# Optimization experiments

Hardware: AMD Instinct MI355X
Metric: run time of the kernel (lower is better)

Reference implementation:

```python
import jax, jax.numpy as jnp
import numpy as np

TOTAL_WORDS = 10000
EMB = 100
SEQ = 80
UNITS = 64


def setup_inputs() -> dict:
    key = jax.random.key(0)
    ks = jax.random.split(key, 10)
    B = 16384
    tokens = jax.random.randint(ks[0], (B, SEQ), 0, TOTAL_WORDS, dtype=jnp.int32)
    s = 0.05
    emb = jax.random.normal(ks[1], (TOTAL_WORDS, EMB), jnp.float32) * s
    Wx0 = jax.random.normal(ks[2], (EMB, UNITS), jnp.float32) * s
    Wh0 = jax.random.normal(ks[3], (UNITS, UNITS), jnp.float32) * s
    b0 = jnp.zeros((UNITS,), jnp.float32)
    Wx1 = jax.random.normal(ks[4], (UNITS, UNITS), jnp.float32) * s
    Wh1 = jax.random.normal(ks[5], (UNITS, UNITS), jnp.float32) * s
    b1 = jnp.zeros((UNITS,), jnp.float32)
    Wout = jax.random.normal(ks[6], (UNITS, 1), jnp.float32) * s
    bout = jnp.zeros((1,), jnp.float32)
    return {"tokens": tokens, "emb": emb, "Wx0": Wx0, "Wh0": Wh0, "b0": b0,
            "Wx1": Wx1, "Wh1": Wh1, "b1": b1, "Wout": Wout, "bout": bout}


def reference(tokens, emb, Wx0, Wh0, b0, Wx1, Wh1, b1, Wout, bout):
    # Embedding lookup: [B, SEQ, EMB]
    x = emb[tokens]
    B = tokens.shape[0]
    # time-major for scan: [SEQ, B, EMB]
    xt = jnp.transpose(x, (1, 0, 2))
    h0 = jnp.zeros((B, UNITS), x.dtype)
    h1 = jnp.zeros((B, UNITS), x.dtype)

    def step(carry, x_t):
        h0, h1 = carry
        # SimpleRNNCell (inference, dropout inactive): h' = tanh(x Wx + h Wh + b)
        h0n = jnp.tanh(x_t @ Wx0 + h0 @ Wh0 + b0)
        h1n = jnp.tanh(h0n @ Wx1 + h1 @ Wh1 + b1)
        return (h0n, h1n), None

    (h0, h1), _ = jax.lax.scan(step, (h0, h1), xt)
    logits = h1 @ Wout + bout  # [B, 1]
    return jax.nn.sigmoid(logits)
```

## Files before the change

kernel.cpp:

```cpp
#include <hip/hip_runtime.h>

#define TOTAL_WORDS 10000
#define EMB 100
#define SEQ 80
#define UNITS 64
#define BATCH 16384


typedef _Float16 f16x8 __attribute__((ext_vector_type(8)));
typedef _Float16 h2    __attribute__((ext_vector_type(2)));
typedef __fp16   fp16x2r __attribute__((ext_vector_type(2)));
typedef float    f32x4 __attribute__((ext_vector_type(4)));
typedef unsigned int u32;
typedef u32      u32x4 __attribute__((ext_vector_type(4)));

#define PIN(x) asm volatile("" : "+v"(x))

__device__ __forceinline__ u32 tanh_pk(float x, float y) {
    h2 v = __builtin_bit_cast(h2, __builtin_amdgcn_cvt_pkrtz(x, y));
    const _Float16 c3 = (_Float16)(-0.33333333f);
    const _Float16 c5 = (_Float16)(0.13333333f);
    h2 x2 = v * v;
    h2 p  = x2 * c5 + c3;
    h2 x3 = x2 * v;
    h2 r  = x3 * p + v;
    return __builtin_bit_cast(u32, r);
}

__device__ __forceinline__ f16x8 tanh_frag(f32x4 a, f32x4 b) {
    u32x4 w;
    w.x = tanh_pk(a[0], a[1]);
    w.y = tanh_pk(a[2], a[3]);
    w.z = tanh_pk(b[0], b[1]);
    w.w = tanh_pk(b[2], b[3]);
    return __builtin_bit_cast(f16x8, w);
}

__global__ void prep_kernel(const float* __restrict__ emb,
                            const float* __restrict__ Wx0,
                            const float* __restrict__ b0,
                            const float* __restrict__ Wh0,
                            const float* __restrict__ Wx1,
                            const float* __restrict__ Wh1,
                            float* __restrict__ embW,
                            _Float16* __restrict__ wfrags) {
    int b = blockIdx.x;
    if (b < 250) {
        __shared__ float wx[EMB * UNITS];
        for (int i = threadIdx.x; i < EMB * UNITS; i += 256)
            wx[i] = Wx0[i];
        __syncthreads();
        const int u = threadIdx.x & 63;
        const int wvi = threadIdx.x >> 6;
        const int vbase = b * 40 + wvi * 10;
        const float bias = b0[u];
        float acc[10];
#pragma unroll
        for (int i = 0; i < 10; ++i) acc[i] = bias;
        const float* er = emb + vbase * EMB;
#pragma unroll 4
        for (int k = 0; k < EMB; ++k) {
            float wxv = wx[k * UNITS + u];
#pragma unroll
            for (int i = 0; i < 10; ++i)
                acc[i] = fmaf(er[i * EMB + k], wxv, acc[i]);
        }
#pragma unroll
        for (int i = 0; i < 10; ++i)
            embW[(vbase + i) * UNITS + u] = acc[i];
    } else {
        int e = (b - 250) * 256 + threadIdx.x;
        int mat = e >> 12;
        int ee = e & 4095;
        int f = ee >> 9;
        int mt = f >> 1, kf = f & 1;
        int rr = ee & 511;
        int l = rr >> 3, j = rr & 7;
        int k = kf * 32 + (l >> 4) * 8 + j;
        int mm = l & 15;
        int col = 32 * (mt >> 1) + 8 * (mm >> 2) + 4 * (mt & 1) + (mm & 3);
        const float* W = (mat == 0) ? Wh0 : (mat == 1) ? Wx1 : Wh1;
        wfrags[e] = (_Float16)W[k * UNITS + col];
    }
}

#define MF(A, B, C) __builtin_amdgcn_mfma_f32_16x16x32_f16(A, B, C, 0, 0, 0)

#define RNN_ITER(EJ, TOK3)                                                    \
    {                                                                         \
                       \
        f32x4 c0 = MF(wh[0][0], h1f0, b1v[0]);                                \
        f32x4 c1 = MF(wh[1][0], h1f0, b1v[1]);                                \
        f32x4 c2 = MF(wh[2][0], h1f0, b1v[2]);                                \
        f32x4 c3 = MF(wh[3][0], h1f0, b1v[3]);                                \
                              \
        f32x4 a0 = MF(w0[0][0], h0f0, EJ[0]);                                 \
        f32x4 a1 = MF(w0[1][0], h0f0, EJ[1]);                                 \
        f32x4 a2 = MF(w0[2][0], h0f0, EJ[2]);                                 \
        f32x4 a3 = MF(w0[3][0], h0f0, EJ[3]);                                 \
                                                        \
        c0 = MF(wh[0][1], h1f1, c0);                                          \
        c1 = MF(wh[1][1], h1f1, c1);                                          \
        c2 = MF(wh[2][1], h1f1, c2);                                          \
        c3 = MF(wh[3][1], h1f1, c3);                                          \
                       \
        {                                                                     \
            const f32x4* pe = embq + (size_t)(TOK3) * 16;                     \
            EJ[0] = pe[0]; EJ[1] = pe[1]; EJ[2] = pe[8]; EJ[3] = pe[9];       \
        }                                                                     \
                                                        \
        a0 = MF(w0[0][1], h0f1, a0);                                          \
        a1 = MF(w0[1][1], h0f1, a1);                                          \
        a2 = MF(w0[2][1], h0f1, a2);                                          \
        a3 = MF(w0[3][1], h0f1, a3);                                          \
                                       \
        c0 = MF(wx[0][0], h0f0, c0);                                          \
        c1 = MF(wx[1][0], h0f0, c1);                                          \
        c2 = MF(wx[2][0], h0f0, c2);                                          \
        c3 = MF(wx[3][0], h0f0, c3);                                          \
                                  \
        f16x8 nh0f0 = tanh_frag(a0, a1);                                      \
        f16x8 nh0f1 = tanh_frag(a2, a3);                                      \
                                       \
        c0 = MF(wx[0][1], h0f1, c0);                                          \
        c1 = MF(wx[1][1], h0f1, c1);                                          \
        c2 = MF(wx[2][1], h0f1, c2);                                          \
        c3 = MF(wx[3][1], h0f1, c3);                                          \
        h0f0 = nh0f0; h0f1 = nh0f1;                                           \
        h1f0 = tanh_frag(c0, c1);                                             \
        h1f1 = tanh_frag(c2, c3);                                             \
    }

__global__ __launch_bounds__(64, 1) void rnn_mfma_kernel(
    const int*      __restrict__ tokens,
    const float*    __restrict__ embW,
    const _Float16* __restrict__ wfrags,
    const float*    __restrict__ b1,
    const float*    __restrict__ Wout,
    const float*    __restrict__ bout,
    float*          __restrict__ out) {
    const int l = threadIdx.x;
    const int q = l >> 4;
    const int n = l & 15;
    const int row0 = blockIdx.x * 16;

    const f16x8* wf8 = (const f16x8*)wfrags;
    f16x8 w0[4][2], wx[4][2], wh[4][2];
#pragma unroll
    for (int t = 0; t < 4; ++t)
#pragma unroll
        for (int kf = 0; kf < 2; ++kf) {
            w0[t][kf] = wf8[(t * 2 + kf) * 64 + l];
            wx[t][kf] = wf8[(8 + t * 2 + kf) * 64 + l];
            wh[t][kf] = wf8[(16 + t * 2 + kf) * 64 + l];
        }

    const f32x4* b1v4 = (const f32x4*)b1;
    f32x4 b1v[4];
    b1v[0] = b1v4[0 + 2 * q];
    b1v[1] = b1v4[1 + 2 * q];
    b1v[2] = b1v4[8 + 2 * q];
    b1v[3] = b1v4[9 + 2 * q];

#pragma unroll
    for (int t = 0; t < 4; ++t) {
        PIN(w0[t][0]); PIN(w0[t][1]);
        PIN(wx[t][0]); PIN(wx[t][1]);
        PIN(wh[t][0]); PIN(wh[t][1]);
        PIN(b1v[t]);
    }

    const f32x4* embq = (const f32x4*)embW + 2 * q;
    const int tokbase = (row0 + n) * SEQ;

    int4 cur = *(const int4*)&tokens[tokbase];
    int4 nxt = *(const int4*)&tokens[tokbase + 4];

    f16x8 h0f0, h0f1, h1f0, h1f1;
    {
        const f32x4* pe = embq + (size_t)cur.x * 16;
        f32x4 p0 = pe[0], p1 = pe[1], p2 = pe[8], p3 = pe[9];
        h0f0 = tanh_frag(p0, p1);
        h0f1 = tanh_frag(p2, p3);
    }
#pragma unroll
    for (int j = 0; j < 8; ++j) { h1f0[j] = (_Float16)0.0f; h1f1[j] = (_Float16)0.0f; }

    f32x4 eA[4], eB[4];
    {
        const f32x4* pe;
        pe = embq + (size_t)cur.y * 16; eA[0]=pe[0]; eA[1]=pe[1]; eA[2]=pe[8]; eA[3]=pe[9];
        pe = embq + (size_t)cur.z * 16; eB[0]=pe[0]; eB[1]=pe[1]; eB[2]=pe[8]; eB[3]=pe[9];
    }

    for (int k = 0; k < SEQ / 4; ++k) {
        int off = (4 * k + 8 <= SEQ - 4) ? (4 * k + 8) : (SEQ - 4);
        int4 nn = *(const int4*)&tokens[tokbase + off];

        RNN_ITER(eA, cur.w)
        RNN_ITER(eB, nxt.x)
        RNN_ITER(eA, nxt.y)
        RNN_ITER(eB, nxt.z)

        cur = nxt;
        nxt = nn;
    }

    {
        f32x4 wo0 = ((const f32x4*)Wout)[2 * q];
        f32x4 wo1 = ((const f32x4*)Wout)[2 * q + 1];
        f32x4 wo2 = ((const f32x4*)Wout)[8 + 2 * q];
        f32x4 wo3 = ((const f32x4*)Wout)[8 + 2 * q + 1];
        float accv = 0.0f;
#pragma unroll
        for (int j = 0; j < 4; ++j) {
            accv = fmaf((float)h1f0[j],     wo0[j], accv);
            accv = fmaf((float)h1f0[4 + j], wo1[j], accv);
            accv = fmaf((float)h1f1[j],     wo2[j], accv);
            accv = fmaf((float)h1f1[4 + j], wo3[j], accv);
        }
        accv += __shfl_down(accv, 16);
        accv += __shfl_down(accv, 32);
        if (l < 16) {
            float z = accv + bout[0];
            out[row0 + n] = 1.0f / (1.0f + __expf(-z));
        }
    }
}

extern "C" void kernel_launch(void* const* d_in, const int* in_sizes, int n_in,
                              void* d_out, int out_size, void* d_ws, size_t ws_size,
                              hipStream_t stream) {
    const int*   tokens = (const int*)d_in[0];
    const float* emb    = (const float*)d_in[1];
    const float* Wx0    = (const float*)d_in[2];
    const float* Wh0    = (const float*)d_in[3];
    const float* b0     = (const float*)d_in[4];
    const float* Wx1    = (const float*)d_in[5];
    const float* Wh1    = (const float*)d_in[6];
    const float* b1     = (const float*)d_in[7];
    const float* Wout   = (const float*)d_in[8];
    const float* bout   = (const float*)d_in[9];
    float* out = (float*)d_out;

    float* embW = (float*)d_ws;
    _Float16* wfrags =
        (_Float16*)((char*)d_ws + (size_t)TOTAL_WORDS * UNITS * 4);

    prep_kernel<<<298, 256, 0, stream>>>(emb, Wx0, b0, Wh0, Wx1, Wh1,
                                         embW, wfrags);
    rnn_mfma_kernel<<<BATCH / 16, 64, 0, stream>>>(tokens, embW, wfrags,
                                                   b1, Wout, bout, out);
}
```

Before: 132.1 us.

## Split layer-1 accumulation into independent chains and deepen embedding prefetch

The layer-1 recurrence is split into two independent MFMA accumulation chains, one for h1·Wh1 with bias and one for h0·Wx1 from zero, which are summed before tanh. The three chains (layer 0, layer-1 recurrent, layer-1 input) are interleaved so consecutive MFMAs do not depend on each other, shortening the dependent chain per step. Embedding prefetch goes from two to four steps ahead using four register buffers, hiding more gather latency at the cost of extra VGPRs and one extra vector add per output.

New measurement: 140.7 us. +6.6%, slower.

```diff
diff --git a/kernel.cpp b/kernel.cpp
--- a/kernel.cpp
+++ b/kernel.cpp
@@ -86,49 +86,45 @@
 
 #define MF(A, B, C) __builtin_amdgcn_mfma_f32_16x16x32_f16(A, B, C, 0, 0, 0)
 
-#define RNN_ITER(EJ, TOK3)                                                    \
+#define RNN_ITER(EJ, TOK5)                                                    \
     {                                                                         \
-                       \
-        f32x4 c0 = MF(wh[0][0], h1f0, b1v[0]);                                \
-        f32x4 c1 = MF(wh[1][0], h1f0, b1v[1]);                                \
-        f32x4 c2 = MF(wh[2][0], h1f0, b1v[2]);                                \
-        f32x4 c3 = MF(wh[3][0], h1f0, b1v[3]);                                \
-                              \
-        f32x4 a0 = MF(w0[0][0], h0f0, EJ[0]);                                 \
-        f32x4 a1 = MF(w0[1][0], h0f0, EJ[1]);                                 \
-        f32x4 a2 = MF(w0[2][0], h0f0, EJ[2]);                                 \
-        f32x4 a3 = MF(w0[3][0], h0f0, EJ[3]);                                 \
-                                                        \
-        c0 = MF(wh[0][1], h1f1, c0);                                          \
-        c1 = MF(wh[1][1], h1f1, c1);                                          \
-        c2 = MF(wh[2][1], h1f1, c2);                                          \
-        c3 = MF(wh[3][1], h1f1, c3);                                          \
+               \
+        f32x4 ch0 = MF(wh[0][0], h1f0, b1v[0]);                               \
+        f32x4 a0  = MF(w0[0][0], h0f0, EJ[0]);                                \
+        f32x4 cx0 = MF(wx[0][0], h0f0, zv);                                   \
+        f32x4 ch1 = MF(wh[1][0], h1f0, b1v[1]);                               \
+        f32x4 a1  = MF(w0[1][0], h0f0, EJ[1]);                                \
+        f32x4 cx1 = MF(wx[1][0], h0f0, zv);                                   \
+        f32x4 ch2 = MF(wh[2][0], h1f0, b1v[2]);                               \
+        f32x4 a2  = MF(w0[2][0], h0f0, EJ[2]);                                \
+        f32x4 cx2 = MF(wx[2][0], h0f0, zv);                                   \
+        f32x4 ch3 = MF(wh[3][0], h1f0, b1v[3]);                               \
+        f32x4 a3  = MF(w0[3][0], h0f0, EJ[3]);                                \
+        f32x4 cx3 = MF(wx[3][0], h0f0, zv);                                   \
+                      \
+        ch0 = MF(wh[0][1], h1f1, ch0);                                        \
+        a0  = MF(w0[0][1], h0f1, a0);                                         \
+        cx0 = MF(wx[0][1], h0f1, cx0);                                        \
+        ch1 = MF(wh[1][1], h1f1, ch1);                                        \
+        a1  = MF(w0[1][1], h0f1, a1);                                         \
+        cx1 = MF(wx[1][1], h0f1, cx1);                                        \
+        ch2 = MF(wh[2][1], h1f1, ch2);                                        \
+        a2  = MF(w0[2][1], h0f1, a2);                                         \
+        cx2 = MF(wx[2][1], h0f1, cx2);                                        \
+        ch3 = MF(wh[3][1], h1f1, ch3);                                        \
+        a3  = MF(w0[3][1], h0f1, a3);                                         \
+        cx3 = MF(wx[3][1], h0f1, cx3);                                        \
                        \
         {                                                                     \
-            const f32x4* pe = embq + (size_t)(TOK3) * 16;                     \
+            const f32x4* pe = embq + (size_t)(TOK5) * 16;                     \
             EJ[0] = pe[0]; EJ[1] = pe[1]; EJ[2] = pe[8]; EJ[3] = pe[9];       \
         }                                                                     \
-                                                        \
-        a0 = MF(w0[0][1], h0f1, a0);                                          \
-        a1 = MF(w0[1][1], h0f1, a1);                                          \
-        a2 = MF(w0[2][1], h0f1, a2);                                          \
-        a3 = MF(w0[3][1], h0f1, a3);                                          \
-                                       \
-        c0 = MF(wx[0][0], h0f0, c0);                                          \
-        c1 = MF(wx[1][0], h0f0, c1);                                          \
-        c2 = MF(wx[2][0], h0f0, c2);                                          \
-        c3 = MF(wx[3][0], h0f0, c3);                                          \
-                                  \
+                 \
         f16x8 nh0f0 = tanh_frag(a0, a1);                                      \
         f16x8 nh0f1 = tanh_frag(a2, a3);                                      \
-                                       \
-        c0 = MF(wx[0][1], h0f1, c0);                                          \
-        c1 = MF(wx[1][1], h0f1, c1);                                          \
-        c2 = MF(wx[2][1], h0f1, c2);                                          \
-        c3 = MF(wx[3][1], h0f1, c3);                                          \
+        h1f0 = tanh_frag(ch0 + cx0, ch1 + cx1);                               \
+        h1f1 = tanh_frag(ch2 + cx2, ch3 + cx3);                               \
         h0f0 = nh0f0; h0f1 = nh0f1;                                           \
-        h1f0 = tanh_frag(c0, c1);                                             \
-        h1f1 = tanh_frag(c2, c3);                                             \
     }
 
 __global__ __launch_bounds__(64, 1) void rnn_mfma_kernel(
@@ -162,6 +158,9 @@
     b1v[2] = b1v4[8 + 2 * q];
     b1v[3] = b1v4[9 + 2 * q];
 
+    f32x4 zv;
+    zv[0] = 0.0f; zv[1] = 0.0f; zv[2] = 0.0f; zv[3] = 0.0f;
+
 #pragma unroll
     for (int t = 0; t < 4; ++t) {
         PIN(w0[t][0]); PIN(w0[t][1]);
@@ -169,6 +168,7 @@
         PIN(wh[t][0]); PIN(wh[t][1]);
         PIN(b1v[t]);
     }
+    PIN(zv);
 
     const f32x4* embq = (const f32x4*)embW + 2 * q;
     const int tokbase = (row0 + n) * SEQ;
@@ -186,21 +186,23 @@
 #pragma unroll
     for (int j = 0; j < 8; ++j) { h1f0[j] = (_Float16)0.0f; h1f1[j] = (_Float16)0.0f; }
 
-    f32x4 eA[4], eB[4];
+    f32x4 e0[4], e1[4], e2[4], e3[4];
     {
         const f32x4* pe;
-        pe = embq + (size_t)cur.y * 16; eA[0]=pe[0]; eA[1]=pe[1]; eA[2]=pe[8]; eA[3]=pe[9];
-        pe = embq + (size_t)cur.z * 16; eB[0]=pe[0]; eB[1]=pe[1]; eB[2]=pe[8]; eB[3]=pe[9];
+        pe = embq + (size_t)cur.y * 16; e0[0]=pe[0]; e0[1]=pe[1]; e0[2]=pe[8]; e0[3]=pe[9];
+        pe = embq + (size_t)cur.z * 16; e1[0]=pe[0]; e1[1]=pe[1]; e1[2]=pe[8]; e1[3]=pe[9];
+        pe = embq + (size_t)cur.w * 16; e2[0]=pe[0]; e2[1]=pe[1]; e2[2]=pe[8]; e2[3]=pe[9];
+        pe = embq + (size_t)nxt.x * 16; e3[0]=pe[0]; e3[1]=pe[1]; e3[2]=pe[8]; e3[3]=pe[9];
     }
 
     for (int k = 0; k < SEQ / 4; ++k) {
         int off = (4 * k + 8 <= SEQ - 4) ? (4 * k + 8) : (SEQ - 4);
         int4 nn = *(const int4*)&tokens[tokbase + off];
 
-        RNN_ITER(eA, cur.w)
-        RNN_ITER(eB, nxt.x)
-        RNN_ITER(eA, nxt.y)
-        RNN_ITER(eB, nxt.z)
+        RNN_ITER(e0, nxt.y)
+        RNN_ITER(e1, nxt.z)
+        RNN_ITER(e2, nxt.w)
+        RNN_ITER(e3, nn.x)
 
         cur = nxt;
         nxt = nn;
```
